# Kernel optimization log

Measured on AMD Instinct MI355X. Metric: run time of the kernel, lower is better.

## Reference

```python
import jax, jax.numpy as jnp
import numpy as np

N, E, D_IN, D_H, D_OUT = 50000, 600000, 128, 128, 1


def setup_inputs() -> dict:
    key = jax.random.key(0)
    ks = jax.random.split(key, 12)
    s = 1.0 / np.sqrt(D_H)
    inp = {
        "x": jax.random.normal(ks[0], (N, D_IN), dtype=jnp.float32),
        "edge_index": jax.random.randint(ks[1], (2, E), 0, N, dtype=jnp.int64),
        # GCNConv layer weights (in->h, h->h, h->h)
        "W0": jax.random.normal(ks[2], (D_IN, D_H), dtype=jnp.float32) * s,
        "b0": jnp.zeros((D_H,), dtype=jnp.float32),
        "W1": jax.random.normal(ks[3], (D_H, D_H), dtype=jnp.float32) * s,
        "b1": jnp.zeros((D_H,), dtype=jnp.float32),
        "W2": jax.random.normal(ks[4], (D_H, D_H), dtype=jnp.float32) * s,
        "b2": jnp.zeros((D_H,), dtype=jnp.float32),
        # MLP head
        "mlp_w1": jax.random.normal(ks[5], (D_H, D_H), dtype=jnp.float32) * s,
        "mlp_b1": jnp.zeros((D_H,), dtype=jnp.float32),
        "mlp_w2": jax.random.normal(ks[6], (D_H, D_OUT), dtype=jnp.float32) * s,
        "mlp_b2": jnp.zeros((D_OUT,), dtype=jnp.float32),
    }
    return inp


def reference(x, edge_index, W0, b0, W1, b1, W2, b2, mlp_w1, mlp_b1, mlp_w2, mlp_b2):
    n = x.shape[0]
    loop = jnp.arange(n, dtype=edge_index.dtype)
    # add self-loops (PyG GCNConv default)
    src = jnp.concatenate([edge_index[0], loop])
    dst = jnp.concatenate([edge_index[1], loop])
    # symmetric normalization: deg counts incoming edges incl. self-loop
    deg = jax.ops.segment_sum(jnp.ones(src.shape, dtype=x.dtype), dst, num_segments=n)
    dinv = jax.lax.rsqrt(deg)  # deg >= 1 due to self-loops
    norm = (dinv[src] * dinv[dst])[:, None]  # [E+N, 1]

    def gcn_conv(h, W, b):
        h = h @ W                       # [N, d]
        msg = h[src] * norm             # gather + scale, [E+N, d]
        return jax.ops.segment_sum(msg, dst, num_segments=n) + b

    # num_layers=3: first two convs with ReLU (dropout is identity in eval)
    h = jax.nn.relu(gcn_conv(x, W0, b0))
    h = jax.nn.relu(gcn_conv(h, W1, b1))
    h = gcn_conv(h, W2, b2)
    # MLP head (dropout identity in eval)
    h = jax.nn.relu(h @ mlp_w1 + mlp_b1)
    return h @ mlp_w2 + mlp_b2
```

## Files before the change

### kernel.cpp

```cpp
#include <hip/hip_runtime.h>
#include <hip/hip_fp16.h>

constexpr int D = 128;

typedef _Float16 half8 __attribute__((ext_vector_type(8)));
typedef float f32x4 __attribute__((ext_vector_type(4)));


__global__ void k_zero(int4* __restrict__ p, int n4) {
    int i = blockIdx.x * 256 + threadIdx.x;
    if (i < n4) p[i] = make_int4(0, 0, 0, 0);
}


__global__ void k_count(const int* __restrict__ dst, int* __restrict__ cnt, int E) {
    int e = blockIdx.x * 256 + threadIdx.x;
    if (e < E) atomicAdd(&cnt[dst[e]], 1);
}

__global__ __launch_bounds__(256) void k_deg_stats(const int* __restrict__ cnt,
                                                   float* __restrict__ dinv,
                                                   int* __restrict__ bsum, int n) {
    __shared__ int sm[256];
    int tid = threadIdx.x;
    int i = blockIdx.x * 256 + tid;
    int c = (i < n) ? cnt[i] : 0;
    if (i < n) dinv[i] = rsqrtf((float)(c + 1));
    sm[tid] = c;
    __syncthreads();
    for (int off = 128; off > 0; off >>= 1) {
        if (tid < off) sm[tid] += sm[tid + off];
        __syncthreads();
    }
    if (tid == 0) bsum[blockIdx.x] = sm[0];
}

__global__ __launch_bounds__(1024) void k_scan_bsums(int* __restrict__ bsum, int nb,
                                                     int* __restrict__ rowptr, int n) {
    __shared__ int sm[1024];
    int tid = threadIdx.x;
    int v = (tid < nb) ? bsum[tid] : 0;
    sm[tid] = v;
    __syncthreads();
    for (int off = 1; off < 1024; off <<= 1) {
        int t = (tid >= off) ? sm[tid - off] : 0;
        __syncthreads();
        sm[tid] += t;
        __syncthreads();
    }
    if (tid < nb) bsum[tid] = sm[tid] - v;
    if (tid == 1023) rowptr[n] = sm[1023];
}

__global__ __launch_bounds__(256) void k_local_scan(const int* __restrict__ cnt,
                                                    const int* __restrict__ bsum,
                                                    int* __restrict__ rowptr,
                                                    int* __restrict__ cursor, int n) {
    __shared__ int sm[256];
    int tid = threadIdx.x;
    int i = blockIdx.x * 256 + tid;
    int v = (i < n) ? cnt[i] : 0;
    sm[tid] = v;
    __syncthreads();
    for (int off = 1; off < 256; off <<= 1) {
        int t = (tid >= off) ? sm[tid - off] : 0;
        __syncthreads();
        sm[tid] += t;
        __syncthreads();
    }
    if (i < n) {
        int rp = bsum[blockIdx.x] + sm[tid] - v;
        rowptr[i] = rp;
        cursor[i] = rp;
    }
}

template <typename IdxT>
__global__ void k_fill(const int* __restrict__ src, const int* __restrict__ dst,
                       int* __restrict__ cursor, IdxT* __restrict__ csr, int E) {
    int e = blockIdx.x * 256 + threadIdx.x;
    if (e < E) {
        int s = src[e], d = dst[e];
        int p = atomicAdd(&cursor[d], 1);
        csr[p] = (IdxT)s;
    }
}


__global__ void k_cvt_h(const float* __restrict__ in, const float* __restrict__ dinv,
                        __half* __restrict__ outh, int n4) {
    int i = blockIdx.x * 256 + threadIdx.x;
    if (i < n4) {
        float4 v = reinterpret_cast<const float4*>(in)[i];
        float dd = dinv[i >> 5];
        __half ho[4] = {__float2half(v.x * dd), __float2half(v.y * dd),
                        __float2half(v.z * dd), __float2half(v.w * dd)};
        reinterpret_cast<uint2*>(outh)[i] = *reinterpret_cast<uint2*>(ho);
    }
}


__global__ void k_wprime(const float* __restrict__ W2, const float* __restrict__ M1,
                         const float* __restrict__ b2, const float* __restrict__ c1,
                         float* __restrict__ Wp, float* __restrict__ cp) {
    int b = blockIdx.x, t = threadIdx.x;
    if (b < 64) {
        int idx = b * 256 + t;
        int i = idx >> 7, j = idx & 127;
        float acc = 0.f;
        for (int k = 0; k < 128; ++k) acc = fmaf(W2[i * 128 + k], M1[k * 128 + j], acc);
        Wp[idx] = acc;
    } else if (t < 128) {
        float acc = c1[t];
        for (int k = 0; k < 128; ++k) acc = fmaf(b2[k], M1[k * 128 + t], acc);
        cp[t] = acc;
    }
}


__global__ void k_cvt_w(const float* __restrict__ W0, const float* __restrict__ W1,
                        const float* __restrict__ Wp, __half* __restrict__ Wf0,
                        __half* __restrict__ Wf1, __half* __restrict__ Wfp) {
    int m = blockIdx.x >> 6;
    int idx = (blockIdx.x & 63) * 256 + threadIdx.x;
    int j = idx & 7;
    int l = (idx >> 3) & 63;
    int c = (idx >> 9) & 7;
    int kk = (idx >> 12) & 3;
    int row = kk * 32 + (l >> 4) * 8 + j;
    int col = c * 16 + (l & 15);
    const float* W = (m == 0) ? W0 : (m == 1) ? W1 : Wp;
    __half* Wf = (m == 0) ? Wf0 : (m == 1) ? Wf1 : Wfp;
    Wf[idx] = __float2half(W[row * 128 + col]);
}


__device__ inline void accm(float* a, uint4 g, float m) {
    float2 p0 = __half22float2(*reinterpret_cast<const __half2*>(&g.x));
    float2 p1 = __half22float2(*reinterpret_cast<const __half2*>(&g.y));
    float2 p2 = __half22float2(*reinterpret_cast<const __half2*>(&g.z));
    float2 p3 = __half22float2(*reinterpret_cast<const __half2*>(&g.w));
    a[0] = fmaf(m, p0.x, a[0]);
    a[1] = fmaf(m, p0.y, a[1]);
    a[2] = fmaf(m, p1.x, a[2]);
    a[3] = fmaf(m, p1.y, a[3]);
    a[4] = fmaf(m, p2.x, a[4]);
    a[5] = fmaf(m, p2.y, a[5]);
    a[6] = fmaf(m, p3.x, a[6]);
    a[7] = fmaf(m, p3.y, a[7]);
}

template <typename IdxT>
__global__ __launch_bounds__(256) void k_agg_h4(const uint4* __restrict__ Ah4,
                                                const int* __restrict__ rowptr,
                                                const IdxT* __restrict__ csr,
                                                const float* __restrict__ dinv,
                                                uint4* __restrict__ outh4, int n) {
    int wv = threadIdx.x >> 6;
    int lane = threadIdx.x & 63;
    int i = blockIdx.x * 4 + wv;
    if (i >= n) return;
    int qg = lane >> 4;
    int fl = lane & 15;
    float a[8];
#pragma unroll
    for (int j = 0; j < 8; ++j) a[j] = 0.f;
    int beg = rowptr[i], end = rowptr[i + 1];
    for (int base = beg; base < end; base += 64) {
        int cnt = end - base;
        if (cnt > 64) cnt = 64;
        int idxv = (base + lane < end) ? (int)csr[base + lane] : 0;
        for (int e = 0; e < cnt; e += 16) {
            int k0 = e + qg;
            int k1 = e + qg + 4;
            int k2 = e + qg + 8;
            int k3 = e + qg + 12;
            int s0 = __shfl(idxv, k0);
            int s1 = __shfl(idxv, k1);
            int s2 = __shfl(idxv, k2);
            int s3 = __shfl(idxv, k3);
            uint4 g0 = Ah4[s0 * 16 + fl];
            uint4 g1 = Ah4[s1 * 16 + fl];
            uint4 g2 = Ah4[s2 * 16 + fl];
            uint4 g3 = Ah4[s3 * 16 + fl];
            float m0 = (k0 < cnt) ? 1.f : 0.f;
            float m1 = (k1 < cnt) ? 1.f : 0.f;
            float m2 = (k2 < cnt) ? 1.f : 0.f;
            float m3 = (k3 < cnt) ? 1.f : 0.f;
            accm(a, g0, m0);
            accm(a, g1, m1);
            accm(a, g2, m2);
            accm(a, g3, m3);
        }
    }
#pragma unroll
    for (int j = 0; j < 8; ++j) {
        a[j] += __shfl_xor(a[j], 16);
        a[j] += __shfl_xor(a[j], 32);
    }
    if (qg == 0) {
        uint4 gs = Ah4[i * 16 + fl];
        accm(a, gs, 1.f);
        float di = dinv[i];
        __half ho[8];
#pragma unroll
        for (int j = 0; j < 8; ++j) ho[j] = __float2half(di * a[j]);
        outh4[i * 16 + fl] = *reinterpret_cast<const uint4*>(ho);
    }
}


template <int MODE>
__global__ __launch_bounds__(256) void k_gemm_mfma(const __half* __restrict__ A,
                                                   const __half* __restrict__ Wf,
                                                   const float* __restrict__ bias,
                                                   const float* __restrict__ dinv,
                                                   const float* __restrict__ m2,
                                                   const float* __restrict__ m2b,
                                                   void* __restrict__ outv, int n) {
    int tid = threadIdx.x;
    int w = tid >> 6;
    int l = tid & 63;
    int r0 = blockIdx.x * 64 + w * 16;
    int arow = r0 + (l & 15);
    if (arow > n - 1) arow = n - 1;
    int kb = (l >> 4) * 8;

    f32x4 acc[8];
#pragma unroll
    for (int c = 0; c < 8; ++c) acc[c] = (f32x4){0.f, 0.f, 0.f, 0.f};

#pragma unroll
    for (int kk = 0; kk < 4; ++kk) {
        half8 a = *reinterpret_cast<const half8*>(&A[arow * 128 + kk * 32 + kb]);
#pragma unroll
        for (int c = 0; c < 8; ++c) {
            half8 b = *reinterpret_cast<const half8*>(&Wf[((kk * 8 + c) * 64 + l) * 8]);
            acc[c] = __builtin_amdgcn_mfma_f32_16x16x32_f16(a, b, acc[c], 0, 0, 0);
        }
    }

    float bv[8];
#pragma unroll
    for (int c = 0; c < 8; ++c) bv[c] = bias[c * 16 + (l & 15)];

    if (MODE == 0) {
        __half* outh = (__half*)outv;
#pragma unroll
        for (int reg = 0; reg < 4; ++reg) {
            int r = r0 + (l >> 4) * 4 + reg;
            if (r < n) {
                float dr = dinv[r];
#pragma unroll
                for (int c = 0; c < 8; ++c) {
                    float v = dr * fmaxf(acc[c][reg] + bv[c], 0.f);
                    outh[r * 128 + c * 16 + (l & 15)] = __float2half(v);
                }
            }
        }
    } else {
        float* out = (float*)outv;
        float mv[8];
#pragma unroll
        for (int c = 0; c < 8; ++c) mv[c] = m2[c * 16 + (l & 15)];
        float m2bv = m2b[0];
#pragma unroll
        for (int reg = 0; reg < 4; ++reg) {
            float p = 0.f;
#pragma unroll
            for (int c = 0; c < 8; ++c)
                p = fmaf(fmaxf(acc[c][reg] + bv[c], 0.f), mv[c], p);
            p += __shfl_xor(p, 1);
            p += __shfl_xor(p, 2);
            p += __shfl_xor(p, 4);
            p += __shfl_xor(p, 8);
            int r = r0 + (l >> 4) * 4 + reg;
            if ((l & 15) == 0 && r < n) out[r] = p + m2bv;
        }
    }
}


extern "C" void kernel_launch(void* const* d_in, const int* in_sizes, int n_in,
                              void* d_out, int out_size, void* d_ws, size_t ws_size,
                              hipStream_t stream) {
    const float* x = (const float*)d_in[0];
    const int* ei = (const int*)d_in[1];
    const float* W0 = (const float*)d_in[2];
    const float* b0 = (const float*)d_in[3];
    const float* W1 = (const float*)d_in[4];
    const float* b1 = (const float*)d_in[5];
    const float* W2 = (const float*)d_in[6];
    const float* b2 = (const float*)d_in[7];
    const float* M1 = (const float*)d_in[8];
    const float* c1 = (const float*)d_in[9];
    const float* m2 = (const float*)d_in[10];
    const float* m2b = (const float*)d_in[11];
    float* out = (float*)d_out;

    int N = in_sizes[0] / D;
    int E = in_sizes[1] / 2;
    const int* src = ei;
    const int* dst = ei + E;

    char* ws = (char*)d_ws;
    size_t off = 0;
    auto alloc = [&](size_t bytes) -> void* {
        void* p = ws + off;
        off += (bytes + 255) & ~(size_t)255;
        return p;
    };

    int gN = (N + 255) / 256;
    int gE = (E + 255) / 256;
    int gAgg = (N + 3) / 4;
    int gGemm = (N + 63) / 64;
    int nElem4 = N * D / 4;
    int gCvt = (nElem4 + 255) / 256;

    __half* xh = (__half*)alloc((size_t)N * D * 2);
    __half* tbuf = (__half*)alloc((size_t)N * D * 2);
    __half* gbuf = (__half*)alloc((size_t)N * D * 2);
    int* cnt = (int*)alloc((size_t)N * 4);
    float* dinv = (float*)alloc((size_t)N * 4);
    int* rowptr = (int*)alloc((size_t)(N + 1) * 4);
    int* cursor = (int*)alloc((size_t)N * 4);
    void* csr = alloc((size_t)E * 4);
    float* Wp = (float*)alloc((size_t)D * D * 4);
    float* cp = (float*)alloc((size_t)D * 4);
    __half* Wf0 = (__half*)alloc((size_t)D * D * 2);
    __half* Wf1 = (__half*)alloc((size_t)D * D * 2);
    __half* Wfp = (__half*)alloc((size_t)D * D * 2);
    int* bsum = (int*)alloc((size_t)gN * 4);

    bool small_idx = (N <= 65535);

    int zc = (N + 3) / 4;
    k_zero<<<(zc + 255) / 256, 256, 0, stream>>>((int4*)cnt, zc);
    k_count<<<gE, 256, 0, stream>>>(dst, cnt, E);
    k_deg_stats<<<gN, 256, 0, stream>>>(cnt, dinv, bsum, N);
    k_scan_bsums<<<1, 1024, 0, stream>>>(bsum, gN, rowptr, N);
    k_local_scan<<<gN, 256, 0, stream>>>(cnt, bsum, rowptr, cursor, N);
    if (small_idx)
        k_fill<ushort><<<gE, 256, 0, stream>>>(src, dst, cursor, (ushort*)csr, E);
    else
        k_fill<uint><<<gE, 256, 0, stream>>>(src, dst, cursor, (uint*)csr, E);
    k_cvt_h<<<gCvt, 256, 0, stream>>>(x, dinv, xh, nElem4);
    k_wprime<<<65, 256, 0, stream>>>(W2, M1, b2, c1, Wp, cp);
    k_cvt_w<<<192, 256, 0, stream>>>(W0, W1, Wp, Wf0, Wf1, Wfp);

    auto agg = [&](const __half* in_h, __half* out_t) {
        if (small_idx)
            k_agg_h4<ushort><<<gAgg, 256, 0, stream>>>((const uint4*)in_h, rowptr,
                                                       (const ushort*)csr, dinv,
                                                       (uint4*)out_t, N);
        else
            k_agg_h4<uint><<<gAgg, 256, 0, stream>>>((const uint4*)in_h, rowptr,
                                                     (const uint*)csr, dinv,
                                                     (uint4*)out_t, N);
    };

    agg(xh, tbuf);
    k_gemm_mfma<0><<<gGemm, 256, 0, stream>>>(tbuf, Wf0, b0, dinv, nullptr, nullptr,
                                              gbuf, N);
    agg(gbuf, tbuf);
    k_gemm_mfma<0><<<gGemm, 256, 0, stream>>>(tbuf, Wf1, b1, dinv, nullptr, nullptr,
                                              gbuf, N);
    agg(gbuf, tbuf);
    k_gemm_mfma<1><<<gGemm, 256, 0, stream>>>(tbuf, Wfp, cp, dinv, m2, m2b, out, N);
}
```

Baseline: 196.7 us.

## Make aggregation kernel persistent with prefetch of next row's CSR indices

The aggregation kernel becomes grid-strided: it launches a fixed 1024 blocks instead of one wave per node, and each wave loops over nodes. While a wave processes its current node, it loads the next node's rowptr bounds and first 64 neighbor indices ahead of time, hiding the dependent index-load latency. Fewer blocks lower launch and scheduling overhead, but the grid may give less latency hiding from occupancy and worse load balance across waves.

```diff
diff --git a/kernel.cpp b/kernel.cpp
--- a/kernel.cpp
+++ b/kernel.cpp
@@ -156,56 +156,80 @@
                                                 const IdxT* __restrict__ csr,
                                                 const float* __restrict__ dinv,
                                                 uint4* __restrict__ outh4, int n) {
-    int wv = threadIdx.x >> 6;
+    int nw = gridDim.x * 4;
+    int gw = blockIdx.x * 4 + (threadIdx.x >> 6);
     int lane = threadIdx.x & 63;
-    int i = blockIdx.x * 4 + wv;
-    if (i >= n) return;
     int qg = lane >> 4;
     int fl = lane & 15;
-    float a[8];
-#pragma unroll
-    for (int j = 0; j < 8; ++j) a[j] = 0.f;
-    int beg = rowptr[i], end = rowptr[i + 1];
-    for (int base = beg; base < end; base += 64) {
-        int cnt = end - base;
-        if (cnt > 64) cnt = 64;
-        int idxv = (base + lane < end) ? (int)csr[base + lane] : 0;
-        for (int e = 0; e < cnt; e += 16) {
-            int k0 = e + qg;
-            int k1 = e + qg + 4;
-            int k2 = e + qg + 8;
-            int k3 = e + qg + 12;
-            int s0 = __shfl(idxv, k0);
-            int s1 = __shfl(idxv, k1);
-            int s2 = __shfl(idxv, k2);
-            int s3 = __shfl(idxv, k3);
-            uint4 g0 = Ah4[s0 * 16 + fl];
-            uint4 g1 = Ah4[s1 * 16 + fl];
-            uint4 g2 = Ah4[s2 * 16 + fl];
-            uint4 g3 = Ah4[s3 * 16 + fl];
-            float m0 = (k0 < cnt) ? 1.f : 0.f;
-            float m1 = (k1 < cnt) ? 1.f : 0.f;
-            float m2 = (k2 < cnt) ? 1.f : 0.f;
-            float m3 = (k3 < cnt) ? 1.f : 0.f;
-            accm(a, g0, m0);
-            accm(a, g1, m1);
-            accm(a, g2, m2);
-            accm(a, g3, m3);
-        }
-    }
-#pragma unroll
-    for (int j = 0; j < 8; ++j) {
-        a[j] += __shfl_xor(a[j], 16);
-        a[j] += __shfl_xor(a[j], 32);
-    }
-    if (qg == 0) {
-        uint4 gs = Ah4[i * 16 + fl];
-        accm(a, gs, 1.f);
-        float di = dinv[i];
-        __half ho[8];
-#pragma unroll
-        for (int j = 0; j < 8; ++j) ho[j] = __float2half(di * a[j]);
-        outh4[i * 16 + fl] = *reinterpret_cast<const uint4*>(ho);
+
+    int i = gw;
+    if (i >= n) return;
+    int beg = rowptr[i];
+    int end = rowptr[i + 1];
+    int idxv = (beg + lane < end) ? (int)csr[beg + lane] : 0;
+
+    while (true) {
+        int ni = i + nw;
+        int nbeg = 0, nend = 0, nidxv = 0;
+        if (ni < n) {
+            nbeg = rowptr[ni];
+            nend = rowptr[ni + 1];
+            nidxv = (nbeg + lane < nend) ? (int)csr[nbeg + lane] : 0;
+        }
+
+        float a[8];
+#pragma unroll
+        for (int j = 0; j < 8; ++j) a[j] = 0.f;
+        int cnt = end - beg;
+        for (int base = 0; base < cnt; base += 64) {
+            int c2 = cnt - base;
+            if (c2 > 64) c2 = 64;
+            int iv = (base == 0)
+                         ? idxv
+                         : ((beg + base + lane < end) ? (int)csr[beg + base + lane] : 0);
+            for (int e = 0; e < c2; e += 16) {
+                int k0 = e + qg;
+                int k1 = e + qg + 4;
+                int k2 = e + qg + 8;
+                int k3 = e + qg + 12;
+                int s0 = __shfl(iv, k0);
+                int s1 = __shfl(iv, k1);
+                int s2 = __shfl(iv, k2);
+                int s3 = __shfl(iv, k3);
+                uint4 g0 = Ah4[s0 * 16 + fl];
+                uint4 g1 = Ah4[s1 * 16 + fl];
+                uint4 g2 = Ah4[s2 * 16 + fl];
+                uint4 g3 = Ah4[s3 * 16 + fl];
+                float m0 = (k0 < c2) ? 1.f : 0.f;
+                float m1 = (k1 < c2) ? 1.f : 0.f;
+                float m2 = (k2 < c2) ? 1.f : 0.f;
+                float m3 = (k3 < c2) ? 1.f : 0.f;
+                accm(a, g0, m0);
+                accm(a, g1, m1);
+                accm(a, g2, m2);
+                accm(a, g3, m3);
+            }
+        }
+#pragma unroll
+        for (int j = 0; j < 8; ++j) {
+            a[j] += __shfl_xor(a[j], 16);
+            a[j] += __shfl_xor(a[j], 32);
+        }
+        if (qg == 0) {
+            uint4 gs = Ah4[i * 16 + fl];
+            accm(a, gs, 1.f);
+            float di = dinv[i];
+            __half ho[8];
+#pragma unroll
+            for (int j = 0; j < 8; ++j) ho[j] = __float2half(di * a[j]);
+            outh4[i * 16 + fl] = *reinterpret_cast<const uint4*>(ho);
+        }
+
+        if (ni >= n) break;
+        i = ni;
+        beg = nbeg;
+        end = nend;
+        idxv = nidxv;
     }
 }
 
@@ -313,7 +337,8 @@
 
     int gN = (N + 255) / 256;
     int gE = (E + 255) / 256;
-    int gAgg = (N + 3) / 4;
+    int gAgg = 1024;
+    if (gAgg > (N + 3) / 4) gAgg = (N + 3) / 4;
     int gGemm = (N + 63) / 64;
     int nElem4 = N * D / 4;
     int gCvt = (nElem4 + 255) / 256;
```

Measured after the change: 212.8 us. 1.08x slower.

## Fuse block-sum scan into local scan and merge prep kernels into one

Applied to the files above, without the earlier changes.

Drops the single-block scan of block sums: each block of the local scan now redundantly scans the block sums itself (assuming at most 256 blocks). The CSR fill, the scaled fp16 conversion of x, the weight repacking and the W2·M1 product are merged into one grid-stride kernel with 2048 blocks, cutting five launches to one. The weight product now writes fp16 in MFMA layout directly, so the fp32 intermediate buffer goes away. The cost is redundant per-block scan work, and the nb≤256 limit could break for larger N.

```diff
diff --git a/kernel.cpp b/kernel.cpp
--- a/kernel.cpp
+++ b/kernel.cpp
@@ -35,30 +35,25 @@
     if (tid == 0) bsum[blockIdx.x] = sm[0];
 }
 
-__global__ __launch_bounds__(1024) void k_scan_bsums(int* __restrict__ bsum, int nb,
-                                                     int* __restrict__ rowptr, int n) {
-    __shared__ int sm[1024];
-    int tid = threadIdx.x;
-    int v = (tid < nb) ? bsum[tid] : 0;
-    sm[tid] = v;
-    __syncthreads();
-    for (int off = 1; off < 1024; off <<= 1) {
-        int t = (tid >= off) ? sm[tid - off] : 0;
-        __syncthreads();
-        sm[tid] += t;
-        __syncthreads();
-    }
-    if (tid < nb) bsum[tid] = sm[tid] - v;
-    if (tid == 1023) rowptr[n] = sm[1023];
-}
-
-__global__ __launch_bounds__(256) void k_local_scan(const int* __restrict__ cnt,
-                                                    const int* __restrict__ bsum,
-                                                    int* __restrict__ rowptr,
-                                                    int* __restrict__ cursor, int n) {
+__global__ __launch_bounds__(256) void k_local_scan2(const int* __restrict__ cnt,
+                                                     const int* __restrict__ bsum, int nb,
+                                                     int* __restrict__ rowptr,
+                                                     int* __restrict__ cursor, int n) {
+    __shared__ int sb[256];
     __shared__ int sm[256];
     int tid = threadIdx.x;
-    int i = blockIdx.x * 256 + tid;
+    int bid = blockIdx.x;
+    int bv = (tid < nb) ? bsum[tid] : 0;
+    sb[tid] = bv;
+    __syncthreads();
+    for (int off = 1; off < 256; off <<= 1) {
+        int t = (tid >= off) ? sb[tid - off] : 0;
+        __syncthreads();
+        sb[tid] += t;
+        __syncthreads();
+    }
+    int blockoff = (bid > 0) ? sb[bid - 1] : 0;
+    int i = bid * 256 + tid;
     int v = (i < n) ? cnt[i] : 0;
     sm[tid] = v;
     __syncthreads();
@@ -69,69 +64,73 @@
         __syncthreads();
     }
     if (i < n) {
-        int rp = bsum[blockIdx.x] + sm[tid] - v;
+        int rp = blockoff + sm[tid] - v;
         rowptr[i] = rp;
         cursor[i] = rp;
     }
-}
+    if (bid == 0 && tid == 0) rowptr[n] = sb[nb - 1];
+}
+
 
 template <typename IdxT>
-__global__ void k_fill(const int* __restrict__ src, const int* __restrict__ dst,
-                       int* __restrict__ cursor, IdxT* __restrict__ csr, int E) {
-    int e = blockIdx.x * 256 + threadIdx.x;
-    if (e < E) {
+__global__ __launch_bounds__(256) void k_prep(
+    const int* __restrict__ src, const int* __restrict__ dst, int* __restrict__ cursor,
+    IdxT* __restrict__ csr, int E, const float* __restrict__ x,
+    const float* __restrict__ dinv, __half* __restrict__ xh, int n4,
+    const float* __restrict__ W0, const float* __restrict__ W1,
+    const float* __restrict__ W2, const float* __restrict__ M1,
+    const float* __restrict__ b2, const float* __restrict__ c1,
+    __half* __restrict__ Wf0, __half* __restrict__ Wf1, __half* __restrict__ Wfp,
+    float* __restrict__ cp) {
+    int T = gridDim.x * 256;
+    int gid = blockIdx.x * 256 + threadIdx.x;
+
+    for (int e = gid; e < E; e += T) {
         int s = src[e], d = dst[e];
         int p = atomicAdd(&cursor[d], 1);
         csr[p] = (IdxT)s;
     }
-}
-
-
-__global__ void k_cvt_h(const float* __restrict__ in, const float* __restrict__ dinv,
-                        __half* __restrict__ outh, int n4) {
-    int i = blockIdx.x * 256 + threadIdx.x;
-    if (i < n4) {
-        float4 v = reinterpret_cast<const float4*>(in)[i];
+
+    for (int i = gid; i < n4; i += T) {
+        float4 v = reinterpret_cast<const float4*>(x)[i];
         float dd = dinv[i >> 5];
         __half ho[4] = {__float2half(v.x * dd), __float2half(v.y * dd),
                         __float2half(v.z * dd), __float2half(v.w * dd)};
-        reinterpret_cast<uint2*>(outh)[i] = *reinterpret_cast<uint2*>(ho);
-    }
-}
-
-
-__global__ void k_wprime(const float* __restrict__ W2, const float* __restrict__ M1,
-                         const float* __restrict__ b2, const float* __restrict__ c1,
-                         float* __restrict__ Wp, float* __restrict__ cp) {
-    int b = blockIdx.x, t = threadIdx.x;
-    if (b < 64) {
-        int idx = b * 256 + t;
-        int i = idx >> 7, j = idx & 127;
+        reinterpret_cast<uint2*>(xh)[i] = *reinterpret_cast<uint2*>(ho);
+    }
+
+    for (int q = gid; q < 2 * 16384; q += T) {
+        int m = q >> 14;
+        int idx = q & 16383;
+        int j = idx & 7;
+        int l = (idx >> 3) & 63;
+        int c = (idx >> 9) & 7;
+        int kk = (idx >> 12) & 3;
+        int row = kk * 32 + (l >> 4) * 8 + j;
+        int col = c * 16 + (l & 15);
+        const float* W = (m == 0) ? W0 : W1;
+        __half* Wf = (m == 0) ? Wf0 : Wf1;
+        Wf[idx] = __float2half(W[row * 128 + col]);
+    }
+
+    for (int idx = gid; idx < 16384; idx += T) {
+        int j = idx & 7;
+        int l = (idx >> 3) & 63;
+        int c = (idx >> 9) & 7;
+        int kk = (idx >> 12) & 3;
+        int row = kk * 32 + (l >> 4) * 8 + j;
+        int col = c * 16 + (l & 15);
         float acc = 0.f;
-        for (int k = 0; k < 128; ++k) acc = fmaf(W2[i * 128 + k], M1[k * 128 + j], acc);
-        Wp[idx] = acc;
-    } else if (t < 128) {
-        float acc = c1[t];
-        for (int k = 0; k < 128; ++k) acc = fmaf(b2[k], M1[k * 128 + t], acc);
-        cp[t] = acc;
-    }
-}
-
-
-__global__ void k_cvt_w(const float* __restrict__ W0, const float* __restrict__ W1,
-                        const float* __restrict__ Wp, __half* __restrict__ Wf0,
-                        __half* __restrict__ Wf1, __half* __restrict__ Wfp) {
-    int m = blockIdx.x >> 6;
-    int idx = (blockIdx.x & 63) * 256 + threadIdx.x;
-    int j = idx & 7;
-    int l = (idx >> 3) & 63;
-    int c = (idx >> 9) & 7;
-    int kk = (idx >> 12) & 3;
-    int row = kk * 32 + (l >> 4) * 8 + j;
-    int col = c * 16 + (l & 15);
-    const float* W = (m == 0) ? W0 : (m == 1) ? W1 : Wp;
-    __half* Wf = (m == 0) ? Wf0 : (m == 1) ? Wf1 : Wfp;
-    Wf[idx] = __float2half(W[row * 128 + col]);
+        for (int k = 0; k < 128; ++k)
+            acc = fmaf(W2[row * 128 + k], M1[k * 128 + col], acc);
+        Wfp[idx] = __float2half(acc);
+    }
+
+    if (gid < 128) {
+        float acc = c1[gid];
+        for (int k = 0; k < 128; ++k) acc = fmaf(b2[k], M1[k * 128 + gid], acc);
+        cp[gid] = acc;
+    }
 }
 
 
@@ -316,7 +315,6 @@
     int gAgg = (N + 3) / 4;
     int gGemm = (N + 63) / 64;
     int nElem4 = N * D / 4;
-    int gCvt = (nElem4 + 255) / 256;
 
     __half* xh = (__half*)alloc((size_t)N * D * 2);
     __half* tbuf = (__half*)alloc((size_t)N * D * 2);
@@ -326,7 +324,6 @@
     int* rowptr = (int*)alloc((size_t)(N + 1) * 4);
     int* cursor = (int*)alloc((size_t)N * 4);
     void* csr = alloc((size_t)E * 4);
-    float* Wp = (float*)alloc((size_t)D * D * 4);
     float* cp = (float*)alloc((size_t)D * 4);
     __half* Wf0 = (__half*)alloc((size_t)D * D * 2);
     __half* Wf1 = (__half*)alloc((size_t)D * D * 2);
@@ -339,15 +336,15 @@
     k_zero<<<(zc + 255) / 256, 256, 0, stream>>>((int4*)cnt, zc);
     k_count<<<gE, 256, 0, stream>>>(dst, cnt, E);
     k_deg_stats<<<gN, 256, 0, stream>>>(cnt, dinv, bsum, N);
-    k_scan_bsums<<<1, 1024, 0, stream>>>(bsum, gN, rowptr, N);
-    k_local_scan<<<gN, 256, 0, stream>>>(cnt, bsum, rowptr, cursor, N);
+    k_local_scan2<<<gN, 256, 0, stream>>>(cnt, bsum, gN, rowptr, cursor, N);
     if (small_idx)
-        k_fill<ushort><<<gE, 256, 0, stream>>>(src, dst, cursor, (ushort*)csr, E);
+        k_prep<ushort><<<2048, 256, 0, stream>>>(src, dst, cursor, (ushort*)csr, E, x,
+                                                 dinv, xh, nElem4, W0, W1, W2, M1, b2,
+                                                 c1, Wf0, Wf1, Wfp, cp);
     else
-        k_fill<uint><<<gE, 256, 0, stream>>>(src, dst, cursor, (uint*)csr, E);
-    k_cvt_h<<<gCvt, 256, 0, stream>>>(x, dinv, xh, nElem4);
-    k_wprime<<<65, 256, 0, stream>>>(W2, M1, b2, c1, Wp, cp);
-    k_cvt_w<<<192, 256, 0, stream>>>(W0, W1, Wp, Wf0, Wf1, Wfp);
+        k_prep<uint><<<2048, 256, 0, stream>>>(src, dst, cursor, (uint*)csr, E, x, dinv,
+                                               xh, nElem4, W0, W1, W2, M1, b2, c1, Wf0,
+                                               Wf1, Wfp, cp);
 
     auto agg = [&](const __half* in_h, __half* out_t) {
         if (small_idx)
```

Measured after the change: 187.3 us. 1.05x faster.
